# Optimization experiments

Measured on AMD Instinct MI355X. Metric: run time of the kernel, lower is better.

Reference implementation:

```python
import jax, jax.numpy as jnp
import numpy as np

_EPS = 1e-5
_NH, _DH = 4, 64  # heads, dim_head


def _ln(x, g, b):
    m = x.mean(-1, keepdims=True)
    v = ((x - m) ** 2).mean(-1, keepdims=True)
    return (x - m) / jnp.sqrt(v + _EPS) * g + b


def _leaky(x):
    return jnp.where(x > 0, x, 0.01 * x)


def _bn_eval(x, g, b):
    # eval-mode BatchNorm with running_mean=0, running_var=1
    return x * (g / np.sqrt(1.0 + _EPS)) + b


def setup_inputs() -> dict:
    key = jax.random.key(0)
    ks = jax.random.split(key, 20)
    B, L, S, D, T, H = 4096, 8, 877, 256, 137, 128
    f = jnp.float32

    def rn(k, shape, s=0.02):
        return jax.random.normal(k, shape, dtype=f) * s

    inp = {}
    inp['source'] = jax.random.normal(ks[0], (B, S), dtype=f)
    inp['source_neighbor'] = jax.random.normal(ks[1], (B, L, S), dtype=f)
    inp['cell_inf'] = jax.random.uniform(ks[2], (B, L + 1, 13), dtype=f)
    # encoder_rna: 877 -> 512 -> 256, Linear+BN(eval)+LeakyReLU
    inp['enc_w1'] = rn(ks[3], (S, 512)); inp['enc_b1'] = jnp.zeros((512,), f)
    inp['enc_bn1_g'] = jnp.ones((512,), f); inp['enc_bn1_b'] = jnp.zeros((512,), f)
    inp['enc_w2'] = rn(ks[4], (512, D)); inp['enc_b2'] = jnp.zeros((D,), f)
    inp['enc_bn2_g'] = jnp.ones((D,), f); inp['enc_bn2_b'] = jnp.zeros((D,), f)
    # projection_rna: Linear(256,256) + LayerNorm + ReLU
    inp['proj_w'] = rn(ks[5], (D, D)); inp['proj_b'] = jnp.zeros((D,), f)
    inp['proj_ln_g'] = jnp.ones((D,), f); inp['proj_ln_b'] = jnp.zeros((D,), f)
    # 1-layer pre-norm transformer (4 heads, dim_head 64, ff_mult 2)
    inp['attn_ln_g'] = jnp.ones((D,), f); inp['attn_ln_b'] = jnp.zeros((D,), f)
    inp['wq'] = rn(ks[6], (D, D)); inp['wk'] = rn(ks[7], (D, D)); inp['wv'] = rn(ks[8], (D, D))
    inp['wo'] = rn(ks[9], (D, D)); inp['wo_b'] = jnp.zeros((D,), f)
    inp['ff_ln_g'] = jnp.ones((D,), f); inp['ff_ln_b'] = jnp.zeros((D,), f)
    inp['ff_w1'] = rn(ks[10], (D, 2 * D)); inp['ff_b1'] = jnp.zeros((2 * D,), f)
    inp['ff_w2'] = rn(ks[11], (2 * D, D)); inp['ff_b2'] = jnp.zeros((D,), f)
    # learned tokens
    inp['token_center'] = rn(ks[12], (1, 1, D))
    inp['token_neigh_1'] = rn(ks[13], (1, 1, D))
    inp['token_neigh_2'] = rn(ks[14], (1, 1, D))
    inp['cell_tokens'] = rn(ks[15], (1, 1, 13, D))
    # 137 independent predict heads, batched: Linear(256,128)+BN+LeakyReLU+Linear(128,1,no bias)
    inp['pred_w1'] = rn(ks[16], (T, D, H)); inp['pred_b1'] = jnp.zeros((T, H), f)
    inp['pred_bn_g'] = jnp.ones((T, H), f); inp['pred_bn_b'] = jnp.zeros((T, H), f)
    inp['pred_w2'] = rn(ks[17], (T, H))
    return inp


def _forward(source, source_neighbor, cell_inf, enc_w1, enc_b1, enc_bn1_g, enc_bn1_b,
             enc_w2, enc_b2, enc_bn2_g, enc_bn2_b, proj_w, proj_b, proj_ln_g, proj_ln_b,
             attn_ln_g, attn_ln_b, wq, wk, wv, wo, wo_b, ff_ln_g, ff_ln_b,
             ff_w1, ff_b1, ff_w2, ff_b2, token_center, token_neigh_1, token_neigh_2,
             cell_tokens, pred_w1, pred_b1, pred_bn_g, pred_bn_b, pred_w2):
    B = source.shape[0]
    x = jnp.concatenate([source[:, None, :], source_neighbor], axis=1)  # [B,N,877]
    N = x.shape[1]
    l = N - 1
    half = l // 2
    valid = jnp.abs(x).sum(-1) > 0                      # [B,N] bool
    vm = valid.astype(x.dtype)[..., None]               # [B,N,1]
    D = token_center.shape[-1]
    # role tokens: center / first-half neigh / second-half neigh, masked
    role = jnp.concatenate([
        token_center,
        jnp.broadcast_to(token_neigh_1, (1, half, D)),
        jnp.broadcast_to(token_neigh_2, (1, l - half, D)),
    ], axis=1) * vm                                      # [B,N,D]
    # class tokens: weighted sum over 13 cell-type tokens, masked
    class_tok = (cell_tokens * cell_inf[..., None]).sum(-2) * vm  # [B,N,D]
    # encoder_rna (dropouts are eval identity)
    h = _leaky(_bn_eval(x @ enc_w1 + enc_b1, enc_bn1_g, enc_bn1_b))
    h = _leaky(_bn_eval(h @ enc_w2 + enc_b2, enc_bn2_g, enc_bn2_b))  # [B,N,D]
    fo = h + role + class_tok
    fo = jax.nn.relu(_ln(fo @ proj_w + proj_b, proj_ln_g, proj_ln_b))
    # local graph transformer encoder (depth=1, pre-norm, masked attention)
    hn = _ln(fo, attn_ln_g, attn_ln_b)
    q = (hn @ wq).reshape(B, N, _NH, _DH)
    k = (hn @ wk).reshape(B, N, _NH, _DH)
    v = (hn @ wv).reshape(B, N, _NH, _DH)
    scores = jnp.einsum('bihd,bjhd->bhij', q, k) * (_DH ** -0.5)
    scores = jnp.where(valid[:, None, None, :], scores, -1e9)
    attn = jax.nn.softmax(scores, axis=-1)
    o = jnp.einsum('bhij,bjhd->bihd', attn, v).reshape(B, N, _NH * _DH)
    fo = fo + o @ wo + wo_b
    hn2 = _ln(fo, ff_ln_g, ff_ln_b)
    fo = fo + jax.nn.gelu(hn2 @ ff_w1 + ff_b1) @ ff_w2 + ff_b2
    feat = fo[:, 0, :]                                   # [B,D] center token
    # 137 predict heads as one batched GEMM + fused BN/LeakyReLU
    ph = jnp.einsum('bd,tdh->bth', feat, pred_w1) + pred_b1   # [B,137,128]
    ph = _leaky(_bn_eval(ph, pred_bn_g, pred_bn_b))
    out = jnp.einsum('bth,th->bt', ph, pred_w2)               # [B,137]
    return out


def reference(source, source_neighbor, cell_inf, enc_w1, enc_b1, enc_bn1_g, enc_bn1_b,
              enc_w2, enc_b2, enc_bn2_g, enc_bn2_b, proj_w, proj_b, proj_ln_g, proj_ln_b,
              attn_ln_g, attn_ln_b, wq, wk, wv, wo, wo_b, ff_ln_g, ff_ln_b,
              ff_w1, ff_b1, ff_w2, ff_b2, token_center, token_neigh_1, token_neigh_2,
              cell_tokens, pred_w1, pred_b1, pred_bn_g, pred_bn_b, pred_w2):
    return _forward(source, source_neighbor, cell_inf, enc_w1, enc_b1, enc_bn1_g, enc_bn1_b,
                    enc_w2, enc_b2, enc_bn2_g, enc_bn2_b, proj_w, proj_b, proj_ln_g, proj_ln_b,
                    attn_ln_g, attn_ln_b, wq, wk, wv, wo, wo_b, ff_ln_g, ff_ln_b,
                    ff_w1, ff_b1, ff_w2, ff_b2, token_center, token_neigh_1, token_neigh_2,
                    cell_tokens, pred_w1, pred_b1, pred_bn_g, pred_bn_b, pred_w2)
```

## Files before the change

### kernel.cpp

```cpp
#include <hip/hip_runtime.h>
#include <hip/hip_bf16.h>
#include <math.h>

typedef __hip_bfloat16 bf16;
typedef __attribute__((ext_vector_type(8))) short short8;
typedef __attribute__((ext_vector_type(4))) float f32x4;

#define BB 4096
#define LL 8
#define NN 9
#define SS 877
#define DD 256
#define D2 512
#define TT 137
#define HH 128
#define MM (BB*NN)
#define KP1 896

__device__ __forceinline__ float lrelu(float x){ return x > 0.f ? x : 0.01f*x; }
__device__ __forceinline__ float gelu_tanh(float x){
    float x3 = x*x*x;
    float t = tanhf(0.7978845608028654f*(x + 0.044715f*x3));
    return 0.5f*x*(1.f + t);
}
__device__ __forceinline__ short f2b(float x){
    union { bf16 h; short s; } u; u.h = __float2bfloat16(x); return u.s;
}
__device__ __forceinline__ float b2f(bf16 v){ return __bfloat162float(v); }

struct SwzD { const float* src; unsigned short* dst; int K; int Nloc; int NBloc;
              int NBt; int nbOff; long long base; };
struct SwzTab { SwzD d[10]; long long total; };

__global__ __launch_bounds__(256) void k_swzall(SwzTab tab){
    for (long long f0 = (long long)blockIdx.x*256 + threadIdx.x; f0 < tab.total;
         f0 += (long long)gridDim.x*256){
        int di = 0;
        #pragma unroll
        for (int q = 1; q < 10; q++) if (f0 >= tab.d[q].base) di = q;
        const SwzD dd = tab.d[di];
        long long f = f0 - dd.base;
        int j = (int)(f & 7); int lane = (int)((f>>3)&63); int h = (int)((f>>9)&7);
        long long u = f>>12;
        int nbl = (int)(u % dd.NBloc), kb = (int)(u / dd.NBloc);
        int k = kb*32 + ((lane>>4)<<3) + j;
        int n = nbl*128 + h*16 + (lane&15);
        float v = (k < dd.K) ? dd.src[(size_t)k*dd.Nloc + n] : 0.f;
        size_t dsti = ((((size_t)kb*dd.NBt + dd.nbOff + nbl)*8 + h)*64 + lane)*8 + j;
        dd.dst[dsti] = (unsigned short)f2b(v);
    }
}

__global__ __launch_bounds__(256) void k_prep(const float* __restrict__ src,
                                              const float* __restrict__ srcn,
                                              float* __restrict__ vm,
                                              unsigned short* __restrict__ xbf){
    int m = blockIdx.x; int b = m / NN, n = m % NN;
    const float* row = (n == 0) ? src + (size_t)b*SS
                                : srcn + ((size_t)b*LL + (n-1))*SS;
    unsigned short* orow = xbf + (size_t)m*KP1;
    float s = 0.f;
    for (int i = threadIdx.x; i < KP1; i += 256){
        float v = (i < SS) ? row[i] : 0.f;
        s += fabsf(v);
        orow[i] = (unsigned short)f2b(v);
    }
    #pragma unroll
    for (int o = 32; o > 0; o >>= 1) s += __shfl_xor(s, o);
    __shared__ float part[4];
    if ((threadIdx.x & 63) == 0) part[threadIdx.x>>6] = s;
    __syncthreads();
    if (threadIdx.x == 0)
        vm[m] = ((part[0]+part[1]+part[2]+part[3]) > 0.f) ? 1.f : 0.f;
}

#define EPI_NONE 0
#define EPI_BN_LEAKY 1
#define EPI_RES 2
#define EPI_GELU 3

__global__ __launch_bounds__(256) void k_mgemm(
    const unsigned short* __restrict__ A, int lda,
    const unsigned short* __restrict__ Wsw, int NBt, int nKb,
    const float* __restrict__ bias, const float* __restrict__ bng,
    const float* __restrict__ bnb, const float* __restrict__ res,
    int res_stride, int mode,
    float* __restrict__ out, bf16* __restrict__ outbf, int ldo)
{
    __shared__ short8 As[2][8][64];
    int row0 = blockIdx.x*128;
    int nb = blockIdx.y;
    int tid = threadIdx.x;
    int wv = tid>>6, lane = tid&63;
    int wr = wv>>1, wc = wv&1, quad = lane>>4, l15 = lane&15;

    f32x4 zz = {0.f,0.f,0.f,0.f};
    f32x4 acc[4][4];
    #pragma unroll
    for (int i=0;i<4;i++){ acc[i][0]=zz; acc[i][1]=zz; acc[i][2]=zz; acc[i][3]=zz; }

    int m0 = tid>>2, k8 = tid&3;
    int dst0 = (m0>>4)*64 + (m0&15) + (k8<<4);
    int dst1 = dst0 + 256;
    const uint4* A0p = (const uint4*)(A + (size_t)(row0+m0)*lda + k8*8);
    const uint4* A1p = (const uint4*)(A + (size_t)(row0+m0+64)*lda + k8*8);
    int ldau4 = lda >> 3;
    (void)ldau4;
    const short8* W8 = (const short8*)Wsw;

    uint4 a1r0, a1r1, a2r0, a2r1;
    short8 w[4], nw[4];

    {
        uint4 x0 = A0p[0], x1 = A1p[0];
        ((uint4*)As[0])[dst0] = x0;
        ((uint4*)As[0])[dst1] = x1;
        a1r0 = A0p[4]; a1r1 = A1p[4];
        #pragma unroll
        for (int h = 0; h < 4; h++)
            w[h] = W8[((size_t)nb*8 + wc*4 + h)*64 + lane];
    }
    for (int kb = 0; kb < nKb; kb++){
        int buf = kb & 1;
        if (kb+2 < nKb){ a2r0 = A0p[(kb+2)*4]; a2r1 = A1p[(kb+2)*4]; }
        if (kb+1 < nKb){
            #pragma unroll
            for (int h = 0; h < 4; h++)
                nw[h] = W8[((size_t)((kb+1)*NBt + nb)*8 + wc*4 + h)*64 + lane];
        }
        __syncthreads();
        short8 afr[4];
        #pragma unroll
        for (int i = 0; i < 4; i++) afr[i] = As[buf][wr*4+i][lane];
        #pragma unroll
        for (int i = 0; i < 4; i++)
            #pragma unroll
            for (int h = 0; h < 4; h++)
                acc[i][h] = __builtin_amdgcn_mfma_f32_16x16x32_bf16(afr[i], w[h], acc[i][h], 0,0,0);
        if (kb+1 < nKb){
            ((uint4*)As[buf^1])[dst0] = a1r0;
            ((uint4*)As[buf^1])[dst1] = a1r1;
            a1r0 = a2r0; a1r1 = a2r1;
            #pragma unroll
            for (int h = 0; h < 4; h++) w[h] = nw[h];
        }
    }

    const float inv = rsqrtf(1.f + 1e-5f);
    #pragma unroll
    for (int i = 0; i < 4; i++){
        int rbase = row0 + wr*64 + i*16 + quad*4;
        #pragma unroll
        for (int h = 0; h < 4; h++){
            int c = nb*128 + wc*64 + h*16 + l15;
            float bi = bias ? bias[c] : 0.f;
            #pragma unroll
            for (int reg = 0; reg < 4; reg++){
                int r = rbase + reg;
                float y = acc[i][h][reg] + bi;
                if (mode == EPI_BN_LEAKY)      y = lrelu(y*(bng[c]*inv) + bnb[c]);
                else if (mode == EPI_RES)      y += res[(size_t)r*res_stride + c];
                else if (mode == EPI_GELU)     y = gelu_tanh(y);
                if (out)   out[(size_t)r*ldo + c] = y;
                if (outbf) outbf[(size_t)r*ldo + c] = __float2bfloat16(y);
            }
        }
    }
}

__global__ __launch_bounds__(256) void k_pred(
    const unsigned short* __restrict__ feat,
    const unsigned short* __restrict__ Wsw,
    const float* __restrict__ b1, const float* __restrict__ bg,
    const float* __restrict__ bb, const float* __restrict__ w2,
    float* __restrict__ outp)
{
    __shared__ short8 As[2][8][64];
    int row0 = blockIdx.x*128;
    int t = blockIdx.y;
    int tid = threadIdx.x;
    int wv = tid>>6, lane = tid&63;
    int quad = lane>>4, l15 = lane&15;

    const float inv = rsqrtf(1.f + 1e-5f);
    float b1v[8], bgv[8], bbv[8], w2v[8];
    #pragma unroll
    for (int h = 0; h < 8; h++){
        int hc = t*HH + h*16 + l15;
        b1v[h] = b1[hc]; bgv[h] = bg[hc]*inv; bbv[h] = bb[hc]; w2v[h] = w2[hc];
    }

    f32x4 zz = {0.f,0.f,0.f,0.f};
    f32x4 acc[2][8];
    #pragma unroll
    for (int i=0;i<2;i++)
        #pragma unroll
        for (int h=0;h<8;h++) acc[i][h] = zz;

    int m0 = tid>>2, k8 = tid&3;
    int dst0 = (m0>>4)*64 + (m0&15) + (k8<<4);
    int dst1 = dst0 + 256;
    const uint4* A0p = (const uint4*)(feat + (size_t)(row0+m0)*DD + k8*8);
    const uint4* A1p = (const uint4*)(feat + (size_t)(row0+m0+64)*DD + k8*8);
    const short8* W8 = (const short8*)Wsw;

    uint4 a1r0, a1r1, a2r0, a2r1;
    short8 w[8], nw[8];
    {
        uint4 x0 = A0p[0], x1 = A1p[0];
        ((uint4*)As[0])[dst0] = x0;
        ((uint4*)As[0])[dst1] = x1;
        a1r0 = A0p[4]; a1r1 = A1p[4];
        #pragma unroll
        for (int h = 0; h < 8; h++)
            w[h] = W8[((size_t)(t*8)*8 + h)*64 + lane];
    }
    for (int kb = 0; kb < 8; kb++){
        int buf = kb & 1;
        if (kb+2 < 8){ a2r0 = A0p[(kb+2)*4]; a2r1 = A1p[(kb+2)*4]; }
        if (kb+1 < 8){
            #pragma unroll
            for (int h = 0; h < 8; h++)
                nw[h] = W8[((size_t)(t*8 + kb+1)*8 + h)*64 + lane];
        }
        __syncthreads();
        short8 afr[2];
        #pragma unroll
        for (int i = 0; i < 2; i++) afr[i] = As[buf][wv*2+i][lane];
        #pragma unroll
        for (int i = 0; i < 2; i++)
            #pragma unroll
            for (int h = 0; h < 8; h++)
                acc[i][h] = __builtin_amdgcn_mfma_f32_16x16x32_bf16(afr[i], w[h], acc[i][h], 0,0,0);
        if (kb+1 < 8){
            ((uint4*)As[buf^1])[dst0] = a1r0;
            ((uint4*)As[buf^1])[dst1] = a1r1;
            a1r0 = a2r0; a1r1 = a2r1;
            #pragma unroll
            for (int h = 0; h < 8; h++) w[h] = nw[h];
        }
    }

    #pragma unroll
    for (int i = 0; i < 2; i++){
        #pragma unroll
        for (int reg = 0; reg < 4; reg++){
            float p = 0.f;
            #pragma unroll
            for (int h = 0; h < 8; h++){
                float y = (acc[i][h][reg] + b1v[h])*bgv[h] + bbv[h];
                p += lrelu(y) * w2v[h];
            }
            p += __shfl_xor(p, 1);
            p += __shfl_xor(p, 2);
            p += __shfl_xor(p, 4);
            p += __shfl_xor(p, 8);
            if (l15 == 0){
                int r = row0 + wv*32 + i*16 + quad*4 + reg;
                outp[(size_t)r*TT + t] = p;
            }
        }
    }
}

__global__ __launch_bounds__(256) void k_rolecls(const float* __restrict__ tokc,
                                                 const float* __restrict__ tokn1,
                                                 const float* __restrict__ tokn2,
                                                 const float* __restrict__ cell_tokens,
                                                 const float* __restrict__ cell_inf,
                                                 const float* __restrict__ vm,
                                                 float* __restrict__ fo,
                                                 bf16* __restrict__ fobf){
    int m = blockIdx.x, d = threadIdx.x;
    int n = m % NN;
    float v = vm[m];
    const float* role = (n == 0) ? tokc : (n <= 4 ? tokn1 : tokn2);
    float cl = 0.f;
    #pragma unroll
    for (int c = 0; c < 13; c++)
        cl += cell_inf[(size_t)m*13 + c] * cell_tokens[c*DD + d];
    float y = fo[(size_t)m*DD + d] + (role[d] + cl) * v;
    fo[(size_t)m*DD + d] = y;
    fobf[(size_t)m*DD + d] = __float2bfloat16(y);
}

__device__ __forceinline__ float blksum(float v, float* part){
    #pragma unroll
    for (int o = 32; o > 0; o >>= 1) v += __shfl_xor(v, o);
    __syncthreads();
    if ((threadIdx.x & 63) == 0) part[threadIdx.x>>6] = v;
    __syncthreads();
    return part[0]+part[1]+part[2]+part[3];
}

__global__ __launch_bounds__(256) void k_lnchain(const float* __restrict__ in,
                                                 const float* __restrict__ g1, const float* __restrict__ b1,
                                                 const float* __restrict__ g2, const float* __restrict__ b2,
                                                 float* __restrict__ fo1, bf16* __restrict__ hn){
    __shared__ float part[4];
    int m = blockIdx.x, d = threadIdx.x;
    float x = in[(size_t)m*DD + d];
    float mu = blksum(x, part) * (1.f/256.f);
    float dx = x - mu;
    float var = blksum(dx*dx, part) * (1.f/256.f);
    float y = dx * rsqrtf(var + 1e-5f) * g1[d] + b1[d];
    y = fmaxf(y, 0.f);
    fo1[(size_t)m*DD + d] = y;
    float mu2 = blksum(y, part) * (1.f/256.f);
    float dy = y - mu2;
    float var2 = blksum(dy*dy, part) * (1.f/256.f);
    hn[(size_t)m*DD + d] = __float2bfloat16(dy * rsqrtf(var2 + 1e-5f) * g2[d] + b2[d]);
}

__global__ __launch_bounds__(256) void k_ln(const float* __restrict__ in,
                                            const float* __restrict__ g, const float* __restrict__ b,
                                            bf16* __restrict__ out){
    __shared__ float part[4];
    int m = blockIdx.x, d = threadIdx.x;
    float x = in[(size_t)m*DD + d];
    float mu = blksum(x, part) * (1.f/256.f);
    float dx = x - mu;
    float var = blksum(dx*dx, part) * (1.f/256.f);
    out[(size_t)m*DD + d] = __float2bfloat16(dx * rsqrtf(var + 1e-5f) * g[d] + b[d]);
}

__global__ __launch_bounds__(256) void k_attn(const bf16* __restrict__ q,
                                              const bf16* __restrict__ kv,
                                              const float* __restrict__ vm,
                                              bf16* __restrict__ o){
    int b = blockIdx.x, t = threadIdx.x;
    __shared__ float ks[NN][DD];
    __shared__ float vs[NN][DD];
    __shared__ float qs[DD];
    __shared__ float sc[4][NN];
    __shared__ float val[NN];
    qs[t] = b2f(q[(size_t)b*DD + t]);
    for (int j = 0; j < NN; j++){
        ks[j][t] = b2f(kv[((size_t)b*NN + j)*D2 + t]);
        vs[j][t] = b2f(kv[((size_t)b*NN + j)*D2 + DD + t]);
    }
    if (t < NN) val[t] = vm[b*NN + t];
    __syncthreads();
    if (t < 4*NN){
        int h = t / NN, j = t % NN;
        float s = 0.f;
        for (int d = 0; d < 64; d++) s += qs[h*64+d] * ks[j][h*64+d];
        s *= 0.125f;
        if (!(val[j] > 0.f)) s = -1e9f;
        sc[h][j] = s;
    }
    __syncthreads();
    if (t < 4){
        float mx = -1e30f;
        for (int j = 0; j < NN; j++) mx = fmaxf(mx, sc[t][j]);
        float den = 0.f;
        for (int j = 0; j < NN; j++){ float e = expf(sc[t][j]-mx); sc[t][j] = e; den += e; }
        float iv = 1.f/den;
        for (int j = 0; j < NN; j++) sc[t][j] *= iv;
    }
    __syncthreads();
    int h = t >> 6;
    float acc = 0.f;
    for (int j = 0; j < NN; j++) acc += sc[h][j] * vs[j][t];
    o[(size_t)b*DD + t] = __float2bfloat16(acc);
}

extern "C" void kernel_launch(void* const* d_in, const int* in_sizes, int n_in,
                              void* d_out, int out_size, void* d_ws, size_t ws_size,
                              hipStream_t stream) {
    const float* src      = (const float*)d_in[0];
    const float* srcn     = (const float*)d_in[1];
    const float* cell_inf = (const float*)d_in[2];
    const float* enc_w1   = (const float*)d_in[3];
    const float* enc_b1   = (const float*)d_in[4];
    const float* bn1g     = (const float*)d_in[5];
    const float* bn1b     = (const float*)d_in[6];
    const float* enc_w2   = (const float*)d_in[7];
    const float* enc_b2   = (const float*)d_in[8];
    const float* bn2g     = (const float*)d_in[9];
    const float* bn2b     = (const float*)d_in[10];
    const float* proj_w   = (const float*)d_in[11];
    const float* proj_b   = (const float*)d_in[12];
    const float* pln_g    = (const float*)d_in[13];
    const float* pln_b    = (const float*)d_in[14];
    const float* aln_g    = (const float*)d_in[15];
    const float* aln_b    = (const float*)d_in[16];
    const float* wq       = (const float*)d_in[17];
    const float* wk       = (const float*)d_in[18];
    const float* wv       = (const float*)d_in[19];
    const float* wo       = (const float*)d_in[20];
    const float* wo_b     = (const float*)d_in[21];
    const float* fln_g    = (const float*)d_in[22];
    const float* fln_b    = (const float*)d_in[23];
    const float* ff_w1    = (const float*)d_in[24];
    const float* ff_b1    = (const float*)d_in[25];
    const float* ff_w2    = (const float*)d_in[26];
    const float* ff_b2    = (const float*)d_in[27];
    const float* tokc     = (const float*)d_in[28];
    const float* tokn1    = (const float*)d_in[29];
    const float* tokn2    = (const float*)d_in[30];
    const float* cell_tok = (const float*)d_in[31];
    const float* pw1      = (const float*)d_in[32];
    const float* pb1      = (const float*)d_in[33];
    const float* pbg      = (const float*)d_in[34];
    const float* pbb      = (const float*)d_in[35];
    const float* pw2      = (const float*)d_in[36];
    float* out            = (float*)d_out;

    char* base = (char*)d_ws;
    size_t off = 0;
    auto alloc = [&](size_t bytes)->char*{
        char* p = base + off;
        off += (bytes + 255) & ~(size_t)255;
        return p;
    };
    bf16* sw_enc1 = (bf16*)alloc((size_t)KP1*D2*2);
    bf16* sw_enc2 = (bf16*)alloc((size_t)D2*DD*2);
    bf16* sw_proj = (bf16*)alloc((size_t)DD*DD*2);
    bf16* sw_wq   = (bf16*)alloc((size_t)DD*DD*2);
    bf16* sw_kv   = (bf16*)alloc((size_t)DD*D2*2);
    bf16* sw_wo   = (bf16*)alloc((size_t)DD*DD*2);
    bf16* sw_ff1  = (bf16*)alloc((size_t)DD*D2*2);
    bf16* sw_ff2  = (bf16*)alloc((size_t)D2*DD*2);
    bf16* sw_pred = (bf16*)alloc((size_t)TT*DD*HH*2);
    float* vm    = (float*)alloc((size_t)MM*4);
    char*  xreg  = alloc((size_t)MM*KP1*2);
    bf16*  h1bf  = (bf16*)alloc((size_t)MM*D2*2);
    float* t0    = (float*)alloc((size_t)MM*DD*4);
    bf16*  hnbf  = (bf16*)alloc((size_t)MM*DD*2);
    bf16*  qbf   = (bf16*)alloc((size_t)BB*DD*2);
    bf16*  obbf  = (bf16*)alloc((size_t)BB*DD*2);
    float* fo2   = (float*)alloc((size_t)BB*DD*4);
    bf16*  hn2bf = (bf16*)alloc((size_t)BB*DD*2);
    bf16*  g1bf  = (bf16*)alloc((size_t)BB*D2*2);
    bf16*  featbf= (bf16*)alloc((size_t)BB*DD*2);
    unsigned short* xbf = (unsigned short*)xreg;
    float* fo   = (float*)xreg;
    bf16*  fobf = (bf16*)(xreg + (size_t)MM*DD*4);
    bf16* kvbf  = h1bf;

    dim3 blk(256);

    SwzTab tab;
    long long cum = 0;
    auto mk = [&](int slot, const float* s, bf16* d, int K, int Kpad, int Nloc,
                  int NBt, int nbOff){
        tab.d[slot] = SwzD{ s, (unsigned short*)d, K, Nloc, Nloc/128, NBt, nbOff, cum };
        cum += (long long)Kpad*Nloc;
    };
    mk(0, enc_w1, sw_enc1, SS, KP1, D2, 4, 0);
    mk(1, enc_w2, sw_enc2, D2, D2, DD, 2, 0);
    mk(2, proj_w, sw_proj, DD, DD, DD, 2, 0);
    mk(3, wq,     sw_wq,   DD, DD, DD, 2, 0);
    mk(4, wk,     sw_kv,   DD, DD, DD, 4, 0);
    mk(5, wv,     sw_kv,   DD, DD, DD, 4, 2);
    mk(6, wo,     sw_wo,   DD, DD, DD, 2, 0);
    mk(7, ff_w1,  sw_ff1,  DD, DD, D2, 4, 0);
    mk(8, ff_w2,  sw_ff2,  D2, D2, DD, 2, 0);
    mk(9, pw1,    sw_pred, TT*DD, TT*DD, HH, 1, 0);
    tab.total = cum;
    k_swzall<<<1024, blk, 0, stream>>>(tab);

    k_prep<<<MM, blk, 0, stream>>>(src, srcn, vm, xbf);

    k_mgemm<<<dim3(MM/128, 4), blk, 0, stream>>>(xbf, KP1,
        (const unsigned short*)sw_enc1, 4, KP1/32, enc_b1, bn1g, bn1b,
        nullptr, 0, EPI_BN_LEAKY, nullptr, h1bf, D2);
    k_mgemm<<<dim3(MM/128, 2), blk, 0, stream>>>((const unsigned short*)h1bf, D2,
        (const unsigned short*)sw_enc2, 2, 16, enc_b2, bn2g, bn2b,
        nullptr, 0, EPI_BN_LEAKY, fo, nullptr, DD);
    k_rolecls<<<MM, blk, 0, stream>>>(tokc, tokn1, tokn2, cell_tok, cell_inf, vm, fo, fobf);
    k_mgemm<<<dim3(MM/128, 2), blk, 0, stream>>>((const unsigned short*)fobf, DD,
        (const unsigned short*)sw_proj, 2, 8, proj_b, nullptr, nullptr,
        nullptr, 0, EPI_NONE, t0, nullptr, DD);
    k_lnchain<<<MM, blk, 0, stream>>>(t0, pln_g, pln_b, aln_g, aln_b, fo, hnbf);
    k_mgemm<<<dim3(MM/128, 4), blk, 0, stream>>>((const unsigned short*)hnbf, DD,
        (const unsigned short*)sw_kv, 4, 8, nullptr, nullptr, nullptr,
        nullptr, 0, EPI_NONE, nullptr, kvbf, D2);
    k_mgemm<<<dim3(BB/128, 2), blk, 0, stream>>>((const unsigned short*)hnbf, NN*DD,
        (const unsigned short*)sw_wq, 2, 8, nullptr, nullptr, nullptr,
        nullptr, 0, EPI_NONE, nullptr, qbf, DD);
    k_attn<<<BB, blk, 0, stream>>>(qbf, kvbf, vm, obbf);
    k_mgemm<<<dim3(BB/128, 2), blk, 0, stream>>>((const unsigned short*)obbf, DD,
        (const unsigned short*)sw_wo, 2, 8, wo_b, nullptr, nullptr,
        fo, NN*DD, EPI_RES, fo2, nullptr, DD);
    k_ln<<<BB, blk, 0, stream>>>(fo2, fln_g, fln_b, hn2bf);
    k_mgemm<<<dim3(BB/128, 4), blk, 0, stream>>>((const unsigned short*)hn2bf, DD,
        (const unsigned short*)sw_ff1, 4, 8, ff_b1, nullptr, nullptr,
        nullptr, 0, EPI_GELU, nullptr, g1bf, D2);
    k_mgemm<<<dim3(BB/128, 2), blk, 0, stream>>>((const unsigned short*)g1bf, D2,
        (const unsigned short*)sw_ff2, 2, 16, ff_b2, nullptr, nullptr,
        fo2, DD, EPI_RES, nullptr, featbf, DD);
    k_pred<<<dim3(BB/128, TT), blk, 0, stream>>>((const unsigned short*)featbf,
        (const unsigned short*)sw_pred, pb1, pbg, pbb, pw2, out);
}
```

Baseline: 780.6 us.

## Swizzle GEMM block order, drop LDS staging in pred kernel, trim dead writes

GEMM launches become 1D grids remapped so groups of 8 row-blocks share an N-block, aiming for better L2 reuse of A and W. The predict-head kernel now reads A fragments directly from global memory instead of double-buffering through shared memory, and removes its barriers. The role/cell kernel no longer writes back the full fp32 features, and the LN chain stores only center-token rows into a compact residual buffer. These cut dead global traffic, but the pred kernel loses its explicit prefetch and may expose load latency.

```diff
diff --git a/kernel.cpp b/kernel.cpp
--- a/kernel.cpp
+++ b/kernel.cpp
@@ -81,15 +81,19 @@
 
 __global__ __launch_bounds__(256) void k_mgemm(
     const unsigned short* __restrict__ A, int lda,
-    const unsigned short* __restrict__ Wsw, int NBt, int nKb,
+    const unsigned short* __restrict__ Wsw, int RB, int NBt, int nKb,
     const float* __restrict__ bias, const float* __restrict__ bng,
     const float* __restrict__ bnb, const float* __restrict__ res,
     int res_stride, int mode,
     float* __restrict__ out, bf16* __restrict__ outbf, int ldo)
 {
     __shared__ short8 As[2][8][64];
-    int row0 = blockIdx.x*128;
-    int nb = blockIdx.y;
+    int id = blockIdx.x;
+    int rbg = RB >> 3;
+    int loc = id >> 3;
+    int rb = (id & 7) + ((loc % rbg) << 3);
+    int nb = loc / rbg;
+    int row0 = rb*128;
     int tid = threadIdx.x;
     int wv = tid>>6, lane = tid&63;
     int wr = wv>>1, wc = wv&1, quad = lane>>4, l15 = lane&15;
@@ -104,8 +108,7 @@
     int dst1 = dst0 + 256;
     const uint4* A0p = (const uint4*)(A + (size_t)(row0+m0)*lda + k8*8);
     const uint4* A1p = (const uint4*)(A + (size_t)(row0+m0+64)*lda + k8*8);
-    int ldau4 = lda >> 3;
-    (void)ldau4;
+    int ldu = lda >> 3;
     const short8* W8 = (const short8*)Wsw;
 
     uint4 a1r0, a1r1, a2r0, a2r1;
@@ -120,6 +123,7 @@
         for (int h = 0; h < 4; h++)
             w[h] = W8[((size_t)nb*8 + wc*4 + h)*64 + lane];
     }
+    (void)ldu;
     for (int kb = 0; kb < nKb; kb++){
         int buf = kb & 1;
         if (kb+2 < nKb){ a2r0 = A0p[(kb+2)*4]; a2r1 = A1p[(kb+2)*4]; }
@@ -175,13 +179,41 @@
     const float* __restrict__ bb, const float* __restrict__ w2,
     float* __restrict__ outp)
 {
-    __shared__ short8 As[2][8][64];
-    int row0 = blockIdx.x*128;
-    int t = blockIdx.y;
+    int id = blockIdx.x;
+    int loc = id >> 3;
+    int t = (id & 7) + ((loc >> 5) << 3);
+    if (t >= TT) return;
+    int row0 = (loc & 31) * 128;
     int tid = threadIdx.x;
     int wv = tid>>6, lane = tid&63;
     int quad = lane>>4, l15 = lane&15;
 
+    f32x4 zz = {0.f,0.f,0.f,0.f};
+    f32x4 acc[2][8];
+    #pragma unroll
+    for (int i=0;i<2;i++)
+        #pragma unroll
+        for (int h=0;h<8;h++) acc[i][h] = zz;
+
+    const short8* W8 = (const short8*)Wsw;
+    const short8* Ap0 = (const short8*)(feat + (size_t)(row0 + wv*32 + l15)*DD + quad*8);
+    const short8* Ap1 = (const short8*)(feat + (size_t)(row0 + wv*32 + 16 + l15)*DD + quad*8);
+
+    #pragma unroll 2
+    for (int kb = 0; kb < 8; kb++){
+        short8 a0 = Ap0[kb*4];
+        short8 a1 = Ap1[kb*4];
+        short8 w[8];
+        #pragma unroll
+        for (int h = 0; h < 8; h++)
+            w[h] = W8[((size_t)(t*8 + kb)*8 + h)*64 + lane];
+        #pragma unroll
+        for (int h = 0; h < 8; h++){
+            acc[0][h] = __builtin_amdgcn_mfma_f32_16x16x32_bf16(a0, w[h], acc[0][h], 0,0,0);
+            acc[1][h] = __builtin_amdgcn_mfma_f32_16x16x32_bf16(a1, w[h], acc[1][h], 0,0,0);
+        }
+    }
+
     const float inv = rsqrtf(1.f + 1e-5f);
     float b1v[8], bgv[8], bbv[8], w2v[8];
     #pragma unroll
@@ -189,58 +221,6 @@
         int hc = t*HH + h*16 + l15;
         b1v[h] = b1[hc]; bgv[h] = bg[hc]*inv; bbv[h] = bb[hc]; w2v[h] = w2[hc];
     }
-
-    f32x4 zz = {0.f,0.f,0.f,0.f};
-    f32x4 acc[2][8];
-    #pragma unroll
-    for (int i=0;i<2;i++)
-        #pragma unroll
-        for (int h=0;h<8;h++) acc[i][h] = zz;
-
-    int m0 = tid>>2, k8 = tid&3;
-    int dst0 = (m0>>4)*64 + (m0&15) + (k8<<4);
-    int dst1 = dst0 + 256;
-    const uint4* A0p = (const uint4*)(feat + (size_t)(row0+m0)*DD + k8*8);
-    const uint4* A1p = (const uint4*)(feat + (size_t)(row0+m0+64)*DD + k8*8);
-    const short8* W8 = (const short8*)Wsw;
-
-    uint4 a1r0, a1r1, a2r0, a2r1;
-    short8 w[8], nw[8];
-    {
-        uint4 x0 = A0p[0], x1 = A1p[0];
-        ((uint4*)As[0])[dst0] = x0;
-        ((uint4*)As[0])[dst1] = x1;
-        a1r0 = A0p[4]; a1r1 = A1p[4];
-        #pragma unroll
-        for (int h = 0; h < 8; h++)
-            w[h] = W8[((size_t)(t*8)*8 + h)*64 + lane];
-    }
-    for (int kb = 0; kb < 8; kb++){
-        int buf = kb & 1;
-        if (kb+2 < 8){ a2r0 = A0p[(kb+2)*4]; a2r1 = A1p[(kb+2)*4]; }
-        if (kb+1 < 8){
-            #pragma unroll
-            for (int h = 0; h < 8; h++)
-                nw[h] = W8[((size_t)(t*8 + kb+1)*8 + h)*64 + lane];
-        }
-        __syncthreads();
-        short8 afr[2];
-        #pragma unroll
-        for (int i = 0; i < 2; i++) afr[i] = As[buf][wv*2+i][lane];
-        #pragma unroll
-        for (int i = 0; i < 2; i++)
-            #pragma unroll
-            for (int h = 0; h < 8; h++)
-                acc[i][h] = __builtin_amdgcn_mfma_f32_16x16x32_bf16(afr[i], w[h], acc[i][h], 0,0,0);
-        if (kb+1 < 8){
-            ((uint4*)As[buf^1])[dst0] = a1r0;
-            ((uint4*)As[buf^1])[dst1] = a1r1;
-            a1r0 = a2r0; a1r1 = a2r1;
-            #pragma unroll
-            for (int h = 0; h < 8; h++) w[h] = nw[h];
-        }
-    }
-
     #pragma unroll
     for (int i = 0; i < 2; i++){
         #pragma unroll
@@ -269,7 +249,7 @@
                                                  const float* __restrict__ cell_tokens,
                                                  const float* __restrict__ cell_inf,
                                                  const float* __restrict__ vm,
-                                                 float* __restrict__ fo,
+                                                 const float* __restrict__ fo,
                                                  bf16* __restrict__ fobf){
     int m = blockIdx.x, d = threadIdx.x;
     int n = m % NN;
@@ -280,7 +260,6 @@
     for (int c = 0; c < 13; c++)
         cl += cell_inf[(size_t)m*13 + c] * cell_tokens[c*DD + d];
     float y = fo[(size_t)m*DD + d] + (role[d] + cl) * v;
-    fo[(size_t)m*DD + d] = y;
     fobf[(size_t)m*DD + d] = __float2bfloat16(y);
 }
 
@@ -296,16 +275,17 @@
 __global__ __launch_bounds__(256) void k_lnchain(const float* __restrict__ in,
                                                  const float* __restrict__ g1, const float* __restrict__ b1,
                                                  const float* __restrict__ g2, const float* __restrict__ b2,
-                                                 float* __restrict__ fo1, bf16* __restrict__ hn){
+                                                 float* __restrict__ fo1c, bf16* __restrict__ hn){
     __shared__ float part[4];
     int m = blockIdx.x, d = threadIdx.x;
+    int b = m / NN; int n = m - b*NN;
     float x = in[(size_t)m*DD + d];
     float mu = blksum(x, part) * (1.f/256.f);
     float dx = x - mu;
     float var = blksum(dx*dx, part) * (1.f/256.f);
     float y = dx * rsqrtf(var + 1e-5f) * g1[d] + b1[d];
     y = fmaxf(y, 0.f);
-    fo1[(size_t)m*DD + d] = y;
+    if (n == 0) fo1c[(size_t)b*DD + d] = y;
     float mu2 = blksum(y, part) * (1.f/256.f);
     float dy = y - mu2;
     float var2 = blksum(dy*dy, part) * (1.f/256.f);
@@ -428,6 +408,7 @@
     bf16*  h1bf  = (bf16*)alloc((size_t)MM*D2*2);
     float* t0    = (float*)alloc((size_t)MM*DD*4);
     bf16*  hnbf  = (bf16*)alloc((size_t)MM*DD*2);
+    float* fo1c  = (float*)alloc((size_t)BB*DD*4);
     bf16*  qbf   = (bf16*)alloc((size_t)BB*DD*2);
     bf16*  obbf  = (bf16*)alloc((size_t)BB*DD*2);
     float* fo2   = (float*)alloc((size_t)BB*DD*4);
@@ -463,34 +444,34 @@
 
     k_prep<<<MM, blk, 0, stream>>>(src, srcn, vm, xbf);
 
-    k_mgemm<<<dim3(MM/128, 4), blk, 0, stream>>>(xbf, KP1,
-        (const unsigned short*)sw_enc1, 4, KP1/32, enc_b1, bn1g, bn1b,
+    k_mgemm<<<dim3((MM/128)*4), blk, 0, stream>>>(xbf, KP1,
+        (const unsigned short*)sw_enc1, MM/128, 4, KP1/32, enc_b1, bn1g, bn1b,
         nullptr, 0, EPI_BN_LEAKY, nullptr, h1bf, D2);
-    k_mgemm<<<dim3(MM/128, 2), blk, 0, stream>>>((const unsigned short*)h1bf, D2,
-        (const unsigned short*)sw_enc2, 2, 16, enc_b2, bn2g, bn2b,
+    k_mgemm<<<dim3((MM/128)*2), blk, 0, stream>>>((const unsigned short*)h1bf, D2,
+        (const unsigned short*)sw_enc2, MM/128, 2, 16, enc_b2, bn2g, bn2b,
         nullptr, 0, EPI_BN_LEAKY, fo, nullptr, DD);
     k_rolecls<<<MM, blk, 0, stream>>>(tokc, tokn1, tokn2, cell_tok, cell_inf, vm, fo, fobf);
-    k_mgemm<<<dim3(MM/128, 2), blk, 0, stream>>>((const unsigned short*)fobf, DD,
-        (const unsigned short*)sw_proj, 2, 8, proj_b, nullptr, nullptr,
+    k_mgemm<<<dim3((MM/128)*2), blk, 0, stream>>>((const unsigned short*)fobf, DD,
+        (const unsigned short*)sw_proj, MM/128, 2, 8, proj_b, nullptr, nullptr,
         nullptr, 0, EPI_NONE, t0, nullptr, DD);
-    k_lnchain<<<MM, blk, 0, stream>>>(t0, pln_g, pln_b, aln_g, aln_b, fo, hnbf);
-    k_mgemm<<<dim3(MM/128, 4), blk, 0, stream>>>((const unsigned short*)hnbf, DD,
-        (const unsigned short*)sw_kv, 4, 8, nullptr, nullptr, nullptr,
+    k_lnchain<<<MM, blk, 0, stream>>>(t0, pln_g, pln_b, aln_g, aln_b, fo1c, hnbf);
+    k_mgemm<<<dim3((MM/128)*4), blk, 0, stream>>>((const unsigned short*)hnbf, DD,
+        (const unsigned short*)sw_kv, MM/128, 4, 8, nullptr, nullptr, nullptr,
         nullptr, 0, EPI_NONE, nullptr, kvbf, D2);
-    k_mgemm<<<dim3(BB/128, 2), blk, 0, stream>>>((const unsigned short*)hnbf, NN*DD,
-        (const unsigned short*)sw_wq, 2, 8, nullptr, nullptr, nullptr,
+    k_mgemm<<<dim3((BB/128)*2), blk, 0, stream>>>((const unsigned short*)hnbf, NN*DD,
+        (const unsigned short*)sw_wq, BB/128, 2, 8, nullptr, nullptr, nullptr,
         nullptr, 0, EPI_NONE, nullptr, qbf, DD);
     k_attn<<<BB, blk, 0, stream>>>(qbf, kvbf, vm, obbf);
-    k_mgemm<<<dim3(BB/128, 2), blk, 0, stream>>>((const unsigned short*)obbf, DD,
-        (const unsigned short*)sw_wo, 2, 8, wo_b, nullptr, nullptr,
-        fo, NN*DD, EPI_RES, fo2, nullptr, DD);
+    k_mgemm<<<dim3((BB/128)*2), blk, 0, stream>>>((const unsigned short*)obbf, DD,
+        (const unsigned short*)sw_wo, BB/128, 2, 8, wo_b, nullptr, nullptr,
+        fo1c, DD, EPI_RES, fo2, nullptr, DD);
     k_ln<<<BB, blk, 0, stream>>>(fo2, fln_g, fln_b, hn2bf);
-    k_mgemm<<<dim3(BB/128, 4), blk, 0, stream>>>((const unsigned short*)hn2bf, DD,
-        (const unsigned short*)sw_ff1, 4, 8, ff_b1, nullptr, nullptr,
+    k_mgemm<<<dim3((BB/128)*4), blk, 0, stream>>>((const unsigned short*)hn2bf, DD,
+        (const unsigned short*)sw_ff1, BB/128, 4, 8, ff_b1, nullptr, nullptr,
         nullptr, 0, EPI_GELU, nullptr, g1bf, D2);
-    k_mgemm<<<dim3(BB/128, 2), blk, 0, stream>>>((const unsigned short*)g1bf, D2,
-        (const unsigned short*)sw_ff2, 2, 16, ff_b2, nullptr, nullptr,
+    k_mgemm<<<dim3((BB/128)*2), blk, 0, stream>>>((const unsigned short*)g1bf, D2,
+        (const unsigned short*)sw_ff2, BB/128, 2, 16, ff_b2, nullptr, nullptr,
         fo2, DD, EPI_RES, nullptr, featbf, DD);
-    k_pred<<<dim3(BB/128, TT), blk, 0, stream>>>((const unsigned short*)featbf,
+    k_pred<<<dim3(8*18*32), blk, 0, stream>>>((const unsigned short*)featbf,
         (const unsigned short*)sw_pred, pb1, pbg, pbb, pw2, out);
 }
```

Result: faster. 757.1 us (-3.0%).
